# Optimization experiments

Measured on AMD Instinct MI355X. Metric: run time of the kernel, lower is better.

The kernel has to match this reference:

```python
import jax, jax.numpy as jnp
import numpy as np

B, L, D_IN, D_OUT = 4, 2048, 4096, 4096


def setup_inputs() -> dict:
    key = jax.random.key(0)
    k1, k2, k3, k4 = jax.random.split(key, 4)
    x = jax.random.normal(k1, (B, L, D_IN), dtype=jnp.float32)
    # base weight stored transposed as [in, out], like self.base = base.T
    base = jax.random.normal(k2, (D_IN, D_OUT), dtype=jnp.float32) * 0.02
    # binary delta sign mask in {0, 1}, stored transposed [in, out]
    mask = jax.random.randint(k3, (D_IN, D_OUT), 0, 2).astype(jnp.int32)
    # coeff = mean(|finetune - base|); a small positive scalar
    coeff = jax.random.uniform(k4, (1,), dtype=jnp.float32) * 0.01
    return {"x": x, "base": base, "coeff": coeff, "mask": mask}


def reference(x, base, coeff, mask):
    # Original: x @ base.T_stored + coeff * (x @ repeated_mask)
    # (t_coeff * x) @ mask == t_coeff * (x @ mask); we avoid materializing the
    # per-batch repeated mask since broadcasting the [in, out] mask is equivalent.
    m = mask.astype(x.dtype)            # {0,1} dequantized mask, [in, out]
    c = coeff[0].astype(x.dtype)
    return jnp.einsum('bld,de->ble', x, base) + c * jnp.einsum('bld,de->ble', x, m)
```

## Files before the change

### kernel.cpp

```cpp
#include <hip/hip_runtime.h>
#include <hip/hip_bf16.h>
#include <stdint.h>

#define DIN 4096
#define DOUT 4096
#define BK 64
#define NT (DIN / BK)

typedef __attribute__((ext_vector_type(8))) short short8;
typedef __attribute__((ext_vector_type(8))) unsigned short ushort8;
typedef __attribute__((ext_vector_type(16))) float f32x16;

__device__ inline unsigned short f2bf(float f) {
    union { float f; unsigned u; } v; v.f = f;
    unsigned r = v.u + 0x7fffu + ((v.u >> 16) & 1u);
    return (unsigned short)(r >> 16);
}


__global__ void cvt_x_blocked(const float* __restrict__ x, ushort* __restrict__ xb) {
    const int t = threadIdx.x;
    const int bx = blockIdx.x;
    const int R = bx >> 6, u = bx & 63;
    const int r32 = t >> 3, kcol = t & 7;
    const int kk = kcol >> 2, s = (kcol >> 1) & 1, h = kcol & 1;
    const float* src = x + ((size_t)R * 256) * DIN + u * 64 + kcol * 8;
    ushort* dst = xb + (size_t)R * 1048576 + (size_t)u * 16384
                + (size_t)kk * 8192 + s * 512 + h * 256 + r32 * 8;
#pragma unroll
    for (int j = 0; j < 8; ++j) {
        const float* p = src + ((size_t)(j * 32 + r32)) * DIN;
        float4 v0 = *(const float4*)p, v1 = *(const float4*)(p + 4);
        ushort8 o;
        o[0] = f2bf(v0.x); o[1] = f2bf(v0.y); o[2] = f2bf(v0.z); o[3] = f2bf(v0.w);
        o[4] = f2bf(v1.x); o[5] = f2bf(v1.y); o[6] = f2bf(v1.z); o[7] = f2bf(v1.w);
        *(ushort8*)(dst + (size_t)j * 1024) = o;
    }
}

__global__ void make_wt_kernel(const float* __restrict__ base, const int* __restrict__ mask,
                               const float* __restrict__ coeff, ushort* __restrict__ wt) {
    __shared__ float tile[64][65];
    const float c = coeff[0];
    const int t = threadIdx.x;
    const int bd = blockIdx.x >> 6;
    const int be = blockIdx.x & 63;
    const int d0 = bd * 64, e0 = be * 64;
#pragma unroll
    for (int i = 0; i < 4; ++i) {
        int idx = i * 256 + t;
        int r = idx >> 4;
        int c4 = (idx & 15) << 2;
        const float4 bv = *(const float4*)(base + (size_t)(d0 + r) * DOUT + e0 + c4);
        const int4  mv = *(const int4*)(mask + (size_t)(d0 + r) * DOUT + e0 + c4);
        tile[r][c4 + 0] = bv.x + c * (float)mv.x;
        tile[r][c4 + 1] = bv.y + c * (float)mv.y;
        tile[r][c4 + 2] = bv.z + c * (float)mv.z;
        tile[r][c4 + 3] = bv.w + c * (float)mv.w;
    }
    __syncthreads();
#pragma unroll
    for (int i = 0; i < 8; ++i) {
        int idx = i * 256 + t;
        int r = idx >> 5;
        int p = (idx & 31) << 1;
        ushort2 o;
        o.x = f2bf(tile[p][r]);
        o.y = f2bf(tile[p + 1][r]);
        *(ushort2*)(wt + (size_t)(e0 + r) * DIN + d0 + p) = o;
    }
}

__global__ void reblock_w(const ushort* __restrict__ wt_rm, ushort* __restrict__ wb) {
    const int t = threadIdx.x;
    const int bx = blockIdx.x;
    const int R = bx >> 6, u = bx & 63;
    const int r32 = t >> 3, kcol = t & 7;
    const int kk = kcol >> 2, s = (kcol >> 1) & 1, h = kcol & 1;
    const ushort* src = wt_rm + ((size_t)R * 256) * DIN + u * 64 + kcol * 8;
    ushort* dst = wb + (size_t)R * 1048576 + (size_t)u * 16384
                + (size_t)kk * 8192 + s * 512 + h * 256 + r32 * 8;
#pragma unroll
    for (int j = 0; j < 8; ++j) {
        ushort8 o = *(const ushort8*)(src + ((size_t)(j * 32 + r32)) * DIN);
        *(ushort8*)(dst + (size_t)j * 1024) = o;
    }
}


#define MFMA32(D, VA, VB) D = __builtin_amdgcn_mfma_f32_32x32x16_bf16(VA, VB, D, 0, 0, 0)

#define GLL(P, L) \
    __builtin_amdgcn_global_load_lds( \
        (const __attribute__((address_space(1))) void*)(P), \
        (__attribute__((address_space(3))) void*)(L), 16, 0, 0)

#define RDA(BUF,KK,MT,S) (*(const short8*)&lA[BUF][KK][awoff + (MT)*1024 + (S)*512])
#define RDB(BUF,KK,NN,S) (*(const short8*)&lB[BUF][KK][bwoff + (NN)*1024 + (S)*512])

#define STAGE_A(BUF,KK,OFE) { GLL(gA0 + (OFE), &lA[BUF][KK][doff]); \
                              GLL(gA1 + (OFE), &lA[BUF][KK][doff + 4096]); }
#define STAGE_B(BUF,KK,OFE) { GLL(gB0 + (OFE), &lB[BUF][KK][doff]); \
                              GLL(gB1 + (OFE), &lB[BUF][KK][doff + 4096]); }

#define WAITV(N)  asm volatile("s_waitcnt vmcnt(" #N ")" ::: "memory")
#define SBAR      __builtin_amdgcn_s_barrier()

#define MFMA8(CX0,CX1,CY0,CY1) \
    MFMA32(CX0, a0s0, b0s0); MFMA32(CX1, a0s0, b1s0); \
    MFMA32(CY0, a1s0, b0s0); MFMA32(CY1, a1s0, b1s0); \
    MFMA32(CX0, a0s1, b0s1); MFMA32(CX1, a0s1, b1s1); \
    MFMA32(CY0, a1s1, b0s1); MFMA32(CY1, a1s1, b1s1);

#define KTILE(BUF, G1, G2, NEXT, OFE1, OFE2) \
  { \
    short8 a0s0,a0s1,a1s0,a1s1,b0s0,b0s1,b1s0,b1s1; \
    a0s0=RDA(BUF,0,0,0); a0s1=RDA(BUF,0,0,1); a1s0=RDA(BUF,0,1,0); a1s1=RDA(BUF,0,1,1); \
    b0s0=RDB(BUF,0,0,0); b0s1=RDB(BUF,0,0,1); b1s0=RDB(BUF,0,1,0); b1s1=RDB(BUF,0,1,1); \
    if (G1) STAGE_A(1-(BUF), 1, OFE1) \
    SBAR; \
    __builtin_amdgcn_s_setprio(1); \
    MFMA8(c00,c01,c10,c11) \
    __builtin_amdgcn_s_setprio(0); \
    WAITV(6); \
    a0s0=RDA(BUF,0,2,0); a0s1=RDA(BUF,0,2,1); a1s0=RDA(BUF,0,3,0); a1s1=RDA(BUF,0,3,1); \
    if (G1) STAGE_B(1-(BUF), 1, OFE1) \
    SBAR; \
    __builtin_amdgcn_s_setprio(1); \
    MFMA8(c20,c21,c30,c31) \
    __builtin_amdgcn_s_setprio(0); \
    a0s0=RDA(BUF,1,0,0); a0s1=RDA(BUF,1,0,1); a1s0=RDA(BUF,1,1,0); a1s1=RDA(BUF,1,1,1); \
    b0s0=RDB(BUF,1,0,0); b0s1=RDB(BUF,1,0,1); b1s0=RDB(BUF,1,1,0); b1s1=RDB(BUF,1,1,1); \
    if (G2) STAGE_A(BUF, 0, OFE2) \
    SBAR; \
    __builtin_amdgcn_s_setprio(1); \
    MFMA8(c00,c01,c10,c11) \
    __builtin_amdgcn_s_setprio(0); \
    a0s0=RDA(BUF,1,2,0); a0s1=RDA(BUF,1,2,1); a1s0=RDA(BUF,1,3,0); a1s1=RDA(BUF,1,3,1); \
    if (G2) STAGE_B(BUF, 0, OFE2) \
    SBAR; \
    __builtin_amdgcn_s_setprio(1); \
    MFMA8(c20,c21,c30,c31) \
    __builtin_amdgcn_s_setprio(0); \
    if (G2)        { WAITV(6); } \
    else if (NEXT) { WAITV(0); } \
    SBAR; \
    __builtin_amdgcn_sched_barrier(0); \
  }

__global__ __launch_bounds__(512, 2) void gemm_kernel(const ushort* __restrict__ A,
                                                      const ushort* __restrict__ Bt,
                                                      float* __restrict__ C) {
    __shared__ __align__(16) ushort lA[2][2][256 * 32];
    __shared__ __align__(16) ushort lB[2][2][256 * 32];

    const int tid = threadIdx.x;
    const int lane = tid & 63;
    const int wave = tid >> 6;

    const int nbn = DOUT / 256;
    const int nwg = gridDim.x;
    int bid = blockIdx.x;
    int cpx = nwg >> 3;
    int s = (bid & 7) * cpx + (bid >> 3);
    const int m0 = (s / nbn) * 256;
    const int n0 = (s % nbn) * 256;

    const int wr = wave >> 2;
    const int wc = wave & 3;
    const int fr = lane & 31;
    const int fq = lane >> 5;

    const int awoff = wr * 4096 + fq * 256 + fr * 8;
    const int bwoff = wc * 2048 + fq * 256 + fr * 8;
    const int doff = tid * 8;

    const ushort* Ablk = A  + (size_t)(m0 >> 8) * 1048576;
    const ushort* Bblk = Bt + (size_t)(n0 >> 8) * 1048576;
    const ushort* gA0 = Ablk + doff;
    const ushort* gA1 = Ablk + doff + 4096;
    const ushort* gB0 = Bblk + doff;
    const ushort* gB1 = Bblk + doff + 4096;

    f32x16 c00 = {}, c01 = {}, c10 = {}, c11 = {};
    f32x16 c20 = {}, c21 = {}, c30 = {}, c31 = {};

    STAGE_A(0, 0, 0)      STAGE_B(0, 0, 0)
    STAGE_A(0, 1, 8192)   STAGE_B(0, 1, 8192)
    STAGE_A(1, 0, 16384)  STAGE_B(1, 0, 16384)
    WAITV(6);
    SBAR;
    __builtin_amdgcn_sched_barrier(0);

    for (int u = 0; u < NT; u += 2) {
        KTILE(0, 1, (u + 2 < NT), 1, 24576, 32768)
        KTILE(1, (u + 2 < NT), (u + 3 < NT), (u + 2 < NT), 40960, 49152)
        gA0 += 32768; gA1 += 32768; gB0 += 32768; gB1 += 32768;
    }

    const int gcb = n0 + wc * 64 + fr;
    const int grb = m0 + wr * 128 + fq * 4;
#define WRT(CT, M32, N32) \
    _Pragma("unroll") \
    for (int r = 0; r < 16; ++r) { \
        int grow = grb + (M32) * 32 + (r & 3) + 8 * (r >> 2); \
        C[(size_t)grow * DOUT + gcb + (N32) * 32] = CT[r]; \
    }
    WRT(c00, 0, 0) WRT(c01, 0, 1) WRT(c10, 1, 0) WRT(c11, 1, 1)
    WRT(c20, 2, 0) WRT(c21, 2, 1) WRT(c30, 3, 0) WRT(c31, 3, 1)
#undef WRT
}

extern "C" void kernel_launch(void* const* d_in, const int* in_sizes, int n_in,
                              void* d_out, int out_size, void* d_ws, size_t ws_size,
                              hipStream_t stream) {
    const float* x = (const float*)d_in[0];
    const float* base = (const float*)d_in[1];
    const float* coeff = (const float*)d_in[2];
    const int* mask = (const int*)d_in[3];
    float* out = (float*)d_out;

    const int M = in_sizes[0] / DIN;
    ushort* xb = (ushort*)d_ws;
    ushort* wb = xb + (size_t)M * DIN;
    ushort* wt_rm = (ushort*)d_out;

    cvt_x_blocked<<<(M / 256) * 64, 256, 0, stream>>>(x, xb);
    make_wt_kernel<<<(DIN / 64) * (DOUT / 64), 256, 0, stream>>>(base, mask, coeff, wt_rm);
    reblock_w<<<(DOUT / 256) * 64, 256, 0, stream>>>(wt_rm, wb);

    const int nwg = (M / 256) * (DOUT / 256);
    gemm_kernel<<<nwg, 512, 0, stream>>>(xb, wb, out);
}
```

Measured before the change: 337.0 us.

## Load A fragments directly into registers and stage only B through LDS

The GEMM main loop is restructured so each wave reads its A operand fragments straight from global memory into registers. Only B is staged through a smaller double-buffered LDS tile, filled by register loads and ds writes instead of global_load_lds. The wave layout changes from 2x4 to 4x2 so each wave owns 64 rows by 128 columns, and the k-step shrinks to 32 with one barrier per step. This cuts LDS traffic and footprint for A, but relies on global and L2 latency for A being hidden by register prefetch one step ahead.

After: 379.2 us. 12.5% more time.

```diff
diff --git a/kernel.cpp b/kernel.cpp
--- a/kernel.cpp
+++ b/kernel.cpp
@@ -4,8 +4,7 @@
 
 #define DIN 4096
 #define DOUT 4096
-#define BK 64
-#define NT (DIN / BK)
+#define NK 128
 
 typedef __attribute__((ext_vector_type(8))) short short8;
 typedef __attribute__((ext_vector_type(8))) unsigned short ushort8;
@@ -90,69 +89,35 @@
 
 #define MFMA32(D, VA, VB) D = __builtin_amdgcn_mfma_f32_32x32x16_bf16(VA, VB, D, 0, 0, 0)
 
-#define GLL(P, L) \
-    __builtin_amdgcn_global_load_lds( \
-        (const __attribute__((address_space(1))) void*)(P), \
-        (__attribute__((address_space(3))) void*)(L), 16, 0, 0)
-
-#define RDA(BUF,KK,MT,S) (*(const short8*)&lA[BUF][KK][awoff + (MT)*1024 + (S)*512])
-#define RDB(BUF,KK,NN,S) (*(const short8*)&lB[BUF][KK][bwoff + (NN)*1024 + (S)*512])
-
-#define STAGE_A(BUF,KK,OFE) { GLL(gA0 + (OFE), &lA[BUF][KK][doff]); \
-                              GLL(gA1 + (OFE), &lA[BUF][KK][doff + 4096]); }
-#define STAGE_B(BUF,KK,OFE) { GLL(gB0 + (OFE), &lB[BUF][KK][doff]); \
-                              GLL(gB1 + (OFE), &lB[BUF][KK][doff + 4096]); }
-
-#define WAITV(N)  asm volatile("s_waitcnt vmcnt(" #N ")" ::: "memory")
-#define SBAR      __builtin_amdgcn_s_barrier()
-
-#define MFMA8(CX0,CX1,CY0,CY1) \
-    MFMA32(CX0, a0s0, b0s0); MFMA32(CX1, a0s0, b1s0); \
-    MFMA32(CY0, a1s0, b0s0); MFMA32(CY1, a1s0, b1s0); \
-    MFMA32(CX0, a0s1, b0s1); MFMA32(CX1, a0s1, b1s1); \
-    MFMA32(CY0, a1s1, b0s1); MFMA32(CY1, a1s1, b1s1);
-
-#define KTILE(BUF, G1, G2, NEXT, OFE1, OFE2) \
+#define RB(P,N,S) (*(const short8*)&lB[P][bw + (N)*1024 + (S)*512])
+
+#define STEP(P, AC, AN, BSW, BSL, AOFF, GW, GA, GL, LOFF) \
   { \
-    short8 a0s0,a0s1,a1s0,a1s1,b0s0,b0s1,b1s0,b1s1; \
-    a0s0=RDA(BUF,0,0,0); a0s1=RDA(BUF,0,0,1); a1s0=RDA(BUF,0,1,0); a1s1=RDA(BUF,0,1,1); \
-    b0s0=RDB(BUF,0,0,0); b0s1=RDB(BUF,0,0,1); b1s0=RDB(BUF,0,1,0); b1s1=RDB(BUF,0,1,1); \
-    if (G1) STAGE_A(1-(BUF), 1, OFE1) \
-    SBAR; \
+    short8 b00=RB(P,0,0),b01=RB(P,0,1),b10=RB(P,1,0),b11=RB(P,1,1); \
+    short8 b20=RB(P,2,0),b21=RB(P,2,1),b30=RB(P,3,0),b31=RB(P,3,1); \
+    if (GA) { AN##0=*(const short8*)(aP+(AOFF));      AN##1=*(const short8*)(aP+(AOFF)+512); \
+              AN##2=*(const short8*)(aP+(AOFF)+1024); AN##3=*(const short8*)(aP+(AOFF)+1536); } \
+    if (GW) { *(short8*)&lB[1-(P)][dw] = BSW##0; *(short8*)&lB[1-(P)][dw+4096] = BSW##1; } \
+    if (GL) { BSL##0 = *(const short8*)(bP+(LOFF)); BSL##1 = *(const short8*)(bP+(LOFF)+4096); } \
     __builtin_amdgcn_s_setprio(1); \
-    MFMA8(c00,c01,c10,c11) \
+    MFMA32(c00, AC##0, b00); MFMA32(c00, AC##1, b01); \
+    MFMA32(c01, AC##0, b10); MFMA32(c01, AC##1, b11); \
+    MFMA32(c02, AC##0, b20); MFMA32(c02, AC##1, b21); \
+    MFMA32(c03, AC##0, b30); MFMA32(c03, AC##1, b31); \
+    MFMA32(c10, AC##2, b00); MFMA32(c10, AC##3, b01); \
+    MFMA32(c11, AC##2, b10); MFMA32(c11, AC##3, b11); \
+    MFMA32(c12, AC##2, b20); MFMA32(c12, AC##3, b21); \
+    MFMA32(c13, AC##2, b30); MFMA32(c13, AC##3, b31); \
     __builtin_amdgcn_s_setprio(0); \
-    WAITV(6); \
-    a0s0=RDA(BUF,0,2,0); a0s1=RDA(BUF,0,2,1); a1s0=RDA(BUF,0,3,0); a1s1=RDA(BUF,0,3,1); \
-    if (G1) STAGE_B(1-(BUF), 1, OFE1) \
-    SBAR; \
-    __builtin_amdgcn_s_setprio(1); \
-    MFMA8(c20,c21,c30,c31) \
-    __builtin_amdgcn_s_setprio(0); \
-    a0s0=RDA(BUF,1,0,0); a0s1=RDA(BUF,1,0,1); a1s0=RDA(BUF,1,1,0); a1s1=RDA(BUF,1,1,1); \
-    b0s0=RDB(BUF,1,0,0); b0s1=RDB(BUF,1,0,1); b1s0=RDB(BUF,1,1,0); b1s1=RDB(BUF,1,1,1); \
-    if (G2) STAGE_A(BUF, 0, OFE2) \
-    SBAR; \
-    __builtin_amdgcn_s_setprio(1); \
-    MFMA8(c00,c01,c10,c11) \
-    __builtin_amdgcn_s_setprio(0); \
-    a0s0=RDA(BUF,1,2,0); a0s1=RDA(BUF,1,2,1); a1s0=RDA(BUF,1,3,0); a1s1=RDA(BUF,1,3,1); \
-    if (G2) STAGE_B(BUF, 0, OFE2) \
-    SBAR; \
-    __builtin_amdgcn_s_setprio(1); \
-    MFMA8(c20,c21,c30,c31) \
-    __builtin_amdgcn_s_setprio(0); \
-    if (G2)        { WAITV(6); } \
-    else if (NEXT) { WAITV(0); } \
-    SBAR; \
+    asm volatile("s_waitcnt lgkmcnt(0)" ::: "memory"); \
+    __builtin_amdgcn_s_barrier(); \
     __builtin_amdgcn_sched_barrier(0); \
   }
 
 __global__ __launch_bounds__(512, 2) void gemm_kernel(const ushort* __restrict__ A,
                                                       const ushort* __restrict__ Bt,
                                                       float* __restrict__ C) {
-    __shared__ __align__(16) ushort lA[2][2][256 * 32];
-    __shared__ __align__(16) ushort lB[2][2][256 * 32];
+    __shared__ __align__(16) ushort lB[2][8192];
 
     const int tid = threadIdx.x;
     const int lane = tid & 63;
@@ -166,48 +131,54 @@
     const int m0 = (s / nbn) * 256;
     const int n0 = (s % nbn) * 256;
 
-    const int wr = wave >> 2;
-    const int wc = wave & 3;
+    const int wr = wave >> 1;
+    const int wc = wave & 1;
     const int fr = lane & 31;
     const int fq = lane >> 5;
 
-    const int awoff = wr * 4096 + fq * 256 + fr * 8;
-    const int bwoff = wc * 2048 + fq * 256 + fr * 8;
-    const int doff = tid * 8;
-
-    const ushort* Ablk = A  + (size_t)(m0 >> 8) * 1048576;
-    const ushort* Bblk = Bt + (size_t)(n0 >> 8) * 1048576;
-    const ushort* gA0 = Ablk + doff;
-    const ushort* gA1 = Ablk + doff + 4096;
-    const ushort* gB0 = Bblk + doff;
-    const ushort* gB1 = Bblk + doff + 4096;
-
-    f32x16 c00 = {}, c01 = {}, c10 = {}, c11 = {};
-    f32x16 c20 = {}, c21 = {}, c30 = {}, c31 = {};
-
-    STAGE_A(0, 0, 0)      STAGE_B(0, 0, 0)
-    STAGE_A(0, 1, 8192)   STAGE_B(0, 1, 8192)
-    STAGE_A(1, 0, 16384)  STAGE_B(1, 0, 16384)
-    WAITV(6);
-    SBAR;
-    __builtin_amdgcn_sched_barrier(0);
-
-    for (int u = 0; u < NT; u += 2) {
-        KTILE(0, 1, (u + 2 < NT), 1, 24576, 32768)
-        KTILE(1, (u + 2 < NT), (u + 3 < NT), (u + 2 < NT), 40960, 49152)
-        gA0 += 32768; gA1 += 32768; gB0 += 32768; gB1 += 32768;
-    }
-
-    const int gcb = n0 + wc * 64 + fr;
-    const int grb = m0 + wr * 128 + fq * 4;
-#define WRT(CT, M32, N32) \
+    const int bw = wc * 4096 + fq * 256 + fr * 8;
+    const int dw = tid * 8;
+
+    const ushort* aP = A + (size_t)(m0 >> 8) * 1048576
+                     + (wr * 2) * 1024 + fq * 256 + fr * 8;
+    const ushort* bP = Bt + (size_t)(n0 >> 8) * 1048576 + tid * 8;
+
+    f32x16 c00 = {}, c01 = {}, c02 = {}, c03 = {};
+    f32x16 c10 = {}, c11 = {}, c12 = {}, c13 = {};
+    short8 aE0, aE1, aE2, aE3, aO0, aO1, aO2, aO3;
+    short8 bsE0, bsE1, bsO0, bsO1;
+
+    {
+        short8 t0 = *(const short8*)(bP);
+        short8 t1 = *(const short8*)(bP + 4096);
+        bsO0 = *(const short8*)(bP + 8192);
+        bsO1 = *(const short8*)(bP + 8192 + 4096);
+        aE0 = *(const short8*)(aP);        aE1 = *(const short8*)(aP + 512);
+        aE2 = *(const short8*)(aP + 1024); aE3 = *(const short8*)(aP + 1536);
+        *(short8*)&lB[0][dw] = t0;
+        *(short8*)&lB[0][dw + 4096] = t1;
+        asm volatile("s_waitcnt lgkmcnt(0)" ::: "memory");
+        __builtin_amdgcn_s_barrier();
+        __builtin_amdgcn_sched_barrier(0);
+    }
+
+    for (int v = 0; v < NK; v += 2) {
+        const bool g = (v < NK - 2);
+        STEP(0, aE, aO, bsO, bsE, 8192, 1, 1, g, 16384)
+        STEP(1, aO, aE, bsE, bsO, 16384, g, g, g, 24576)
+        aP += 16384; bP += 16384;
+    }
+
+    const int gcb = n0 + wc * 128 + fr;
+    const int grb = m0 + wr * 64 + fq * 4;
+#define WRT(CT, MT, NN) \
     _Pragma("unroll") \
     for (int r = 0; r < 16; ++r) { \
-        int grow = grb + (M32) * 32 + (r & 3) + 8 * (r >> 2); \
-        C[(size_t)grow * DOUT + gcb + (N32) * 32] = CT[r]; \
-    }
-    WRT(c00, 0, 0) WRT(c01, 0, 1) WRT(c10, 1, 0) WRT(c11, 1, 1)
-    WRT(c20, 2, 0) WRT(c21, 2, 1) WRT(c30, 3, 0) WRT(c31, 3, 1)
+        int grow = grb + (MT) * 32 + (r & 3) + 8 * (r >> 2); \
+        C[(size_t)grow * DOUT + gcb + (NN) * 32] = CT[r]; \
+    }
+    WRT(c00, 0, 0) WRT(c01, 0, 1) WRT(c02, 0, 2) WRT(c03, 0, 3)
+    WRT(c10, 1, 0) WRT(c11, 1, 1) WRT(c12, 1, 2) WRT(c13, 1, 3)
 #undef WRT
 }
 
```
